# Performance work log

Hardware: AMD Instinct MI355X
Metric: run time of the kernel (lower is better)

Reference implementation:

```python
import jax, jax.numpy as jnp
import numpy as np

E = 8          # num_experts
K = 2          # top-k
H = 768        # hidden_size
F = 4 * H      # FFN intermediate (expansion_factor=4)
B, S = 2, 2048


def setup_inputs() -> dict:
    key = jax.random.key(0)
    ks = jax.random.split(key, 5)
    scale = 0.02
    return {
        "x": jax.random.normal(ks[0], (B, S, H), dtype=jnp.float32),
        "router_w": jax.random.normal(ks[1], (H, E), dtype=jnp.float32) * scale,
        "router_b": jnp.zeros((E,), dtype=jnp.float32),
        "w1": jax.random.normal(ks[2], (E, H, F), dtype=jnp.float32) * scale,
        "b1": jnp.zeros((E, F), dtype=jnp.float32),
        "w2": jax.random.normal(ks[3], (E, F, H), dtype=jnp.float32) * scale,
        "b2": jnp.zeros((E, H), dtype=jnp.float32),
    }


def reference(x, router_w, router_b, w1, b1, w2, b2):
    b, s, h = x.shape
    # Router
    scores = jnp.einsum("bsh,he->bse", x, router_w) + router_b
    probs = jax.nn.softmax(scores, axis=-1)                      # [b,s,E]
    top_probs, expert_ids = jax.lax.top_k(probs, K)              # [b,s,K]

    # Load-balance auxiliary loss (Switch-style)
    avg_probs = probs.mean(axis=(0, 1))                          # [E]
    top1 = jnp.argmax(probs, axis=-1).reshape(-1)                # [b*s]
    counts = jnp.zeros((E,), dtype=probs.dtype).at[top1].add(1.0)
    expert_freqs = counts / (b * s)
    bal_loss = 0.001 * jnp.dot(expert_freqs, avg_probs)

    # Normalize top-k gate weights
    norm_probs = top_probs / (top_probs.sum(axis=-1, keepdims=True) + 1e-9)  # [b,s,K]

    # Expert FFNs with ReLU^2 activation, computed per-expert (dense, then masked)
    h1 = jnp.einsum("bsh,ehf->ebsf", x, w1) + b1[:, None, None, :]
    h1 = jnp.square(jax.nn.relu(h1))
    h2 = jnp.einsum("ebsf,efh->ebsh", h1, w2) + b2[:, None, None, :]  # [E,b,s,H]

    # Combine: weight for expert e at token (b,s) = sum_k norm_probs * 1[ids_k == e]
    onehot = jax.nn.one_hot(expert_ids, E, dtype=x.dtype)        # [b,s,K,E]
    gate = jnp.einsum("bsk,bske->ebs", norm_probs, onehot)       # [E,b,s]
    out = jnp.einsum("ebs,ebsh->bsh", gate, h2)                  # [b,s,H]
    return out, bal_loss
```

## Files before the change

### kernel.cpp

```cpp
#include <hip/hip_runtime.h>
#include <hip/hip_bf16.h>
#include <stdint.h>

#define E_EXP 8
#define TOK   4096
#define HD    768
#define FD    3072
#define BK    64
#define CAP   8320

typedef __attribute__((ext_vector_type(8))) short bf16x8;
typedef __attribute__((ext_vector_type(4))) float f32x4;

__device__ __forceinline__ unsigned short f2bf(float f) {
  union { float f; unsigned u; } v; v.f = f;
  unsigned r = v.u + 0x7fffu + ((v.u >> 16) & 1u);
  return (unsigned short)(r >> 16);
}
__device__ __forceinline__ float bf2f(unsigned short u) {
  union { unsigned u; float f; } v; v.u = ((unsigned)u) << 16;
  return v.f;
}

__device__ __forceinline__ void gload_lds16(const void* g, void* l) {
  __builtin_amdgcn_global_load_lds(
      (const __attribute__((address_space(1))) unsigned int*)g,
      (__attribute__((address_space(3))) unsigned int*)l, 16, 0, 0);
}

__device__ __forceinline__ int xcd_swizzle(int orig, int nwg) {
  int xcd = orig & 7, base = orig >> 3;
  int q = nwg >> 3, r = nwg & 7;
  return (xcd < r ? xcd * (q + 1) : r * (q + 1) + (xcd - r) * q) + base;
}

__global__ __launch_bounds__(256) void router_kernel(
    const float* __restrict__ x, const float* __restrict__ rw,
    const float* __restrict__ rb, unsigned short* __restrict__ xb,
    float* __restrict__ probs, int* __restrict__ ids,
    float* __restrict__ gates)
{
  __shared__ float lrw[E_EXP * HD];
  for (int i = threadIdx.x; i < E_EXP * HD; i += 256) {
    int h = i >> 3, e = i & 7;
    lrw[e * HD + h] = rw[i];
  }
  __syncthreads();
  const int wave = threadIdx.x >> 6, lane = threadIdx.x & 63;
  const int t = blockIdx.x * 4 + wave;
  const float* xrow = x + (size_t)t * HD;
  float acc[8] = {0, 0, 0, 0, 0, 0, 0, 0};
#pragma unroll
  for (int i = 0; i < HD / 64; ++i) {
    int h = i * 64 + lane;
    float xv = xrow[h];
    xb[(size_t)t * HD + h] = f2bf(xv);
#pragma unroll
    for (int e = 0; e < 8; ++e) acc[e] += xv * lrw[e * HD + h];
  }
#pragma unroll
  for (int d = 1; d < 64; d <<= 1) {
#pragma unroll
    for (int e = 0; e < 8; ++e) acc[e] += __shfl_xor(acc[e], d);
  }
  if (lane == 0) {
    float p[8]; float m = -1e30f, sum = 0.f;
#pragma unroll
    for (int e = 0; e < 8; ++e) { p[e] = acc[e] + rb[e]; m = fmaxf(m, p[e]); }
#pragma unroll
    for (int e = 0; e < 8; ++e) { p[e] = __expf(p[e] - m); sum += p[e]; }
    float inv = 1.f / sum;
#pragma unroll
    for (int e = 0; e < 8; ++e) p[e] *= inv;
    int i1 = 0;
#pragma unroll
    for (int e = 1; e < 8; ++e) if (p[e] > p[i1]) i1 = e;
    int i2 = (i1 == 0) ? 1 : 0;
#pragma unroll
    for (int e = 0; e < 8; ++e) if (e != i1 && p[e] > p[i2]) i2 = e;
    ids[t * 2] = i1; ids[t * 2 + 1] = i2;
    float den = 1.f / (p[i1] + p[i2] + 1e-9f);
    gates[t * 2] = p[i1] * den; gates[t * 2 + 1] = p[i2] * den;
#pragma unroll
    for (int e = 0; e < 8; ++e) probs[t * 8 + e] = p[e];
  }
}

#define W1_TILES (E_EXP * (FD / 32) * (HD / 32))
#define W2_TILES (E_EXP * (HD / 32) * (FD / 32))
__global__ __launch_bounds__(256) void transpose_kernel(
    const float* __restrict__ w1, unsigned short* __restrict__ w1t,
    const float* __restrict__ w2, unsigned short* __restrict__ w2t)
{
  __shared__ float tile[32][33];
  int id = blockIdx.x;
  const float* W; unsigned short* Wt; int Kd, Nd;
  if (id < W1_TILES) {
    W = w1; Wt = w1t; Kd = HD; Nd = FD;
  } else {
    id -= W1_TILES; W = w2; Wt = w2t; Kd = FD; Nd = HD;
  }
  const int nx = Nd / 32;
  const int e = id / (nx * (Kd / 32));
  const int rem = id % (nx * (Kd / 32));
  const int n0 = (rem % nx) * 32, k0 = (rem / nx) * 32;

  const int ci = threadIdx.x & 31, ri = threadIdx.x >> 5;
  const float* src = W + ((size_t)e * Kd + k0) * Nd + n0;
#pragma unroll
  for (int i = 0; i < 32; i += 8)
    tile[ri + i][ci] = src[(size_t)(ri + i) * Nd + ci];
  __syncthreads();
  unsigned short* dst = Wt + ((size_t)e * Nd + n0) * Kd + k0;
  const int co = (threadIdx.x & 15) * 2, ro = threadIdx.x >> 4;
#pragma unroll
  for (int i = 0; i < 32; i += 16) {
    int r = ro + i;
    unsigned v = (unsigned)f2bf(tile[co][r]) | ((unsigned)f2bf(tile[co + 1][r]) << 16);
    *(unsigned*)&dst[(size_t)r * Kd + co] = v;
  }
}

__global__ __launch_bounds__(256) void stats_kernel(
    const int* __restrict__ ids, const float* __restrict__ probs,
    int* __restrict__ meta, float* __restrict__ loss_out)
{
  __shared__ int cnt[8], top1c[8];
  __shared__ float wsum[4][8];
  if (threadIdx.x < 8) { cnt[threadIdx.x] = 0; top1c[threadIdx.x] = 0; }
  __syncthreads();
  float local[8] = {0, 0, 0, 0, 0, 0, 0, 0};
  for (int t = threadIdx.x; t < TOK; t += 256) {
    int e0 = ids[2 * t], e1 = ids[2 * t + 1];
    atomicAdd(&cnt[e0], 1); atomicAdd(&cnt[e1], 1); atomicAdd(&top1c[e0], 1);
    const float4* pr = (const float4*)&probs[(size_t)t * 8];
    float4 a = pr[0], b = pr[1];
    local[0] += a.x; local[1] += a.y; local[2] += a.z; local[3] += a.w;
    local[4] += b.x; local[5] += b.y; local[6] += b.z; local[7] += b.w;
  }
#pragma unroll
  for (int d = 1; d < 64; d <<= 1) {
#pragma unroll
    for (int e = 0; e < 8; ++e) local[e] += __shfl_xor(local[e], d);
  }
  const int wave = threadIdx.x >> 6, lane = threadIdx.x & 63;
  if (lane == 0) {
#pragma unroll
    for (int e = 0; e < 8; ++e) wsum[wave][e] = local[e];
  }
  __syncthreads();
  if (threadIdx.x == 0) {
    int total = 0, nt1 = 0;
    for (int e = 0; e < 8; ++e) {
      int c = cnt[e];
      meta[e] = c;
      meta[16 + e] = total;
      int t1 = (c + 127) >> 7;
      for (int i = 0; i < t1; ++i) { meta[64 + nt1 * 2] = e; meta[64 + nt1 * 2 + 1] = total + i * 128; ++nt1; }
      total += c;
    }
    meta[32] = nt1;
    float loss = 0.f;
    for (int e = 0; e < 8; ++e) {
      float psum = wsum[0][e] + wsum[1][e] + wsum[2][e] + wsum[3][e];
      loss += ((float)top1c[e] / 4096.f) * (psum / 4096.f);
    }
    loss_out[0] = 0.001f * loss;
  }
}

__global__ __launch_bounds__(256) void scatter_kernel(
    const int* __restrict__ ids, int* __restrict__ meta,
    int* __restrict__ token_list, int* __restrict__ pos_list)
{
  __shared__ int lcnt[8];
  __shared__ int lbase[8];
  if (threadIdx.x < 8) lcnt[threadIdx.x] = 0;
  __syncthreads();
  const int t = blockIdx.x * 256 + threadIdx.x;
  const int e0 = ids[t * 2], e1 = ids[t * 2 + 1];
  const int s0 = atomicAdd(&lcnt[e0], 1);
  const int s1 = atomicAdd(&lcnt[e1], 1);
  __syncthreads();
  if (threadIdx.x < 8)
    lbase[threadIdx.x] = atomicAdd(&meta[24 + threadIdx.x], lcnt[threadIdx.x]);
  __syncthreads();
  int p0 = meta[16 + e0] + lbase[e0] + s0;
  int p1 = meta[16 + e1] + lbase[e1] + s1;
  token_list[p0] = t; pos_list[t * 2] = p0;
  token_list[p1] = t; pos_list[t * 2 + 1] = p1;
}

template<int BM, int BN, int MODE, int NW, int NKP>
__global__ __launch_bounds__(NW * 64, 4) void moe_gemm(
    const unsigned short* __restrict__ A,
    const unsigned short* __restrict__ Bw,
    const float* __restrict__ bias,
    const int* __restrict__ token_list,
    const int* __restrict__ meta,
    unsigned short* __restrict__ Cout,
    const int Kdim, const int NN)
{
  const int NY = NN / BN;
  const int wgid = xcd_swizzle(blockIdx.x, gridDim.x);
  const int mt = wgid / (NY * NKP);
  const int slot = wgid - mt * (NY * NKP);
  const int ny = slot % NY;
  const int kp = slot / NY;
  const int nt_total = meta[32];
  if (mt >= nt_total) return;
  const int* tmap = meta + 64;
  const int e = tmap[mt * 2], arow0 = tmap[mt * 2 + 1];
  const int ne_end = meta[16 + e] + meta[e];
  const int n0 = ny * BN;
  const int KLEN = Kdim / NKP;
  const int kbeg = kp * KLEN;
  unsigned short* Cp = Cout + (size_t)kp * CAP * NN;

  __shared__ unsigned short lA[BM * BK];
  __shared__ unsigned short lB[BN * BK];

  const int tid = threadIdx.x;
  const int wave = tid >> 6, lane = tid & 63;
  constexpr int WC_N = NW / 2;
  const int wr = wave / WC_N, wc = wave % WC_N;
  constexpr int WROWS = BM / 2;
  constexpr int WCOLS = BN / WC_N;
  constexpr int FM = WROWS / 16, FN = WCOLS / 16;
  constexpr int NCA = (BM / 8) / NW;
  constexpr int NCB = (BN / 8) / NW;

  const int kswz = ((lane & 7) ^ ((lane >> 3) & 7)) * 8;

  size_t aSrc[NCA];
#pragma unroll
  for (int i = 0; i < NCA; ++i) {
    int c = wave + i * NW;
    int r = c * 8 + (lane >> 3);
    int grow = (MODE == 0) ? token_list[arow0 + r] : (arow0 + r);
    aSrc[i] = (size_t)grow * Kdim + kbeg + kswz;
  }
  size_t bSrc[NCB];
#pragma unroll
  for (int i = 0; i < NCB; ++i) {
    int c = wave + i * NW;
    int n = n0 + c * 8 + (lane >> 3);
    bSrc[i] = ((size_t)e * NN + n) * Kdim + kbeg + kswz;
  }

  f32x4 acc[FM][FN] = {};

  for (int k0 = 0; k0 < KLEN; k0 += BK) {
#pragma unroll
    for (int i = 0; i < NCA; ++i)
      gload_lds16(A + aSrc[i] + k0, &lA[(wave + i * NW) * 512]);
#pragma unroll
    for (int i = 0; i < NCB; ++i)
      gload_lds16(Bw + bSrc[i] + k0, &lB[(wave + i * NW) * 512]);
    __syncthreads();
#pragma unroll
    for (int kk = 0; kk < BK; kk += 32) {
      bf16x8 af[FM], bfr[FN];
      const int lc = (kk >> 3) + (lane >> 4);
#pragma unroll
      for (int m2 = 0; m2 < FM; ++m2) {
        int row = wr * WROWS + m2 * 16 + (lane & 15);
        af[m2] = *(const bf16x8*)&lA[row * BK + ((lc ^ (row & 7)) << 3)];
      }
#pragma unroll
      for (int n2 = 0; n2 < FN; ++n2) {
        int row = wc * WCOLS + n2 * 16 + (lane & 15);
        bfr[n2] = *(const bf16x8*)&lB[row * BK + ((lc ^ (row & 7)) << 3)];
      }
#pragma unroll
      for (int m2 = 0; m2 < FM; ++m2)
#pragma unroll
        for (int n2 = 0; n2 < FN; ++n2)
          acc[m2][n2] = __builtin_amdgcn_mfma_f32_16x16x32_bf16(
              af[m2], bfr[n2], acc[m2][n2], 0, 0, 0);
    }
    __syncthreads();
  }

  const float* be = bias + (size_t)e * NN;
#pragma unroll
  for (int m2 = 0; m2 < FM; ++m2) {
    const int lr = wr * WROWS + m2 * 16 + (lane >> 4) * 4;
#pragma unroll
    for (int n2 = 0; n2 < FN; ++n2) {
      const int col = n0 + wc * WCOLS + n2 * 16 + (lane & 15);
      const float bv = (kp == 0) ? be[col] : 0.f;
#pragma unroll
      for (int j = 0; j < 4; ++j) {
        const int arow = arow0 + lr + j;
        if (arow < ne_end) {
          float v = acc[m2][n2][j] + bv;
          if (MODE == 0) { v = fmaxf(v, 0.f); v = v * v; }
          Cp[(size_t)arow * NN + col] = f2bf(v);
        }
      }
    }
  }
}

__global__ __launch_bounds__(256) void combine_kernel(
    const unsigned short* __restrict__ h2, const int* __restrict__ pos_list,
    const float* __restrict__ gates, float* __restrict__ out)
{
  const unsigned short* h2b = h2 + (size_t)CAP * HD;
  const int wave = threadIdx.x >> 6, lane = threadIdx.x & 63;
  const int t = blockIdx.x * 4 + wave;
  const int p0 = pos_list[2 * t], p1 = pos_list[2 * t + 1];
  const float g0 = gates[2 * t], g1 = gates[2 * t + 1];
  const unsigned short* r0a = h2  + (size_t)p0 * HD;
  const unsigned short* r0b = h2b + (size_t)p0 * HD;
  const unsigned short* r1a = h2  + (size_t)p1 * HD;
  const unsigned short* r1b = h2b + (size_t)p1 * HD;
  float* o = out + (size_t)t * HD;
#pragma unroll
  for (int i = 0; i < 3; ++i) {
    int h = i * 256 + lane * 4;
    ushort4 a0 = *(const ushort4*)&r0a[h];
    ushort4 b0 = *(const ushort4*)&r0b[h];
    ushort4 a1 = *(const ushort4*)&r1a[h];
    ushort4 b1 = *(const ushort4*)&r1b[h];
    float4 o4;
    o4.x = g0 * (bf2f(a0.x) + bf2f(b0.x)) + g1 * (bf2f(a1.x) + bf2f(b1.x));
    o4.y = g0 * (bf2f(a0.y) + bf2f(b0.y)) + g1 * (bf2f(a1.y) + bf2f(b1.y));
    o4.z = g0 * (bf2f(a0.z) + bf2f(b0.z)) + g1 * (bf2f(a1.z) + bf2f(b1.z));
    o4.w = g0 * (bf2f(a0.w) + bf2f(b0.w)) + g1 * (bf2f(a1.w) + bf2f(b1.w));
    *(float4*)&o[h] = o4;
  }
}

extern "C" void kernel_launch(void* const* d_in, const int* in_sizes, int n_in,
                              void* d_out, int out_size, void* d_ws, size_t ws_size,
                              hipStream_t stream)
{
  (void)in_sizes; (void)n_in; (void)ws_size; (void)out_size;
  const float* x  = (const float*)d_in[0];
  const float* rw = (const float*)d_in[1];
  const float* rb = (const float*)d_in[2];
  const float* w1 = (const float*)d_in[3];
  const float* b1 = (const float*)d_in[4];
  const float* w2 = (const float*)d_in[5];
  const float* b2 = (const float*)d_in[6];
  float* out = (float*)d_out;

  char* ws = (char*)d_ws;
  size_t off = 0;
  auto alloc = [&](size_t bytes) {
    off = (off + 255) & ~(size_t)255;
    void* p = ws + off;
    off += bytes;
    return p;
  };
  unsigned short* xb  = (unsigned short*)alloc((size_t)TOK * HD * 2);
  unsigned short* w1t = (unsigned short*)alloc((size_t)E_EXP * FD * HD * 2);
  unsigned short* w2t = (unsigned short*)alloc((size_t)E_EXP * HD * FD * 2);
  unsigned short* h1  = (unsigned short*)alloc((size_t)CAP * FD * 2);
  unsigned short* h2  = (unsigned short*)alloc((size_t)2 * CAP * HD * 2);
  int*   token_list = (int*)alloc(CAP * 4);
  int*   pos_list   = (int*)alloc((size_t)TOK * 2 * 4);
  int*   ids        = (int*)alloc((size_t)TOK * 2 * 4);
  float* gates      = (float*)alloc((size_t)TOK * 2 * 4);
  float* probs      = (float*)alloc((size_t)TOK * 8 * 4);
  int*   meta       = (int*)alloc(1024 * 4);
  char*  ctrl       = (char*)token_list;
  size_t ctrl_bytes = (ws + off) - ctrl;

  hipMemsetAsync(ctrl, 0, ctrl_bytes, stream);

  router_kernel<<<TOK / 4, 256, 0, stream>>>(x, rw, rb, xb, probs, ids, gates);
  transpose_kernel<<<W1_TILES + W2_TILES, 256, 0, stream>>>(w1, w1t, w2, w2t);
  stats_kernel<<<1, 256, 0, stream>>>(ids, probs, meta, out + (size_t)TOK * HD);
  scatter_kernel<<<TOK / 256, 256, 0, stream>>>(ids, meta, token_list, pos_list);
  moe_gemm<128, 128, 0, 4, 1><<<71 * (FD / 128), 256, 0, stream>>>(
      xb, w1t, b1, token_list, meta, h1, HD, FD);
  moe_gemm<128, 128, 1, 4, 2><<<71 * (HD / 128) * 2, 256, 0, stream>>>(
      h1, w2t, b2, token_list, meta, h2, FD, HD);
  combine_kernel<<<TOK / 4, 256, 0, stream>>>(h2, pos_list, gates, out);
}
```

Baseline: 201.8 us.

## Double-buffer LDS tiles in grouped expert GEMM to overlap loads with MFMA

Splits the A and B LDS tiles into two buffers and restructures the K loop so the global-to-LDS load for the next tile is issued before the MFMA work on the current tile. One barrier per iteration, preceded by an explicit vmcnt wait, replaces the two __syncthreads. The goal is to hide global memory latency behind matrix math. In exchange LDS use per block doubles, which can lower occupancy, and skipping the compiler's lgkmcnt wait before the barrier risks a read/write race on the buffer being refilled.

After: 255.5 us. 1.27x slower.

```diff
diff --git a/kernel.cpp b/kernel.cpp
--- a/kernel.cpp
+++ b/kernel.cpp
@@ -217,8 +217,8 @@
   const int kbeg = kp * KLEN;
   unsigned short* Cp = Cout + (size_t)kp * CAP * NN;
 
-  __shared__ unsigned short lA[BM * BK];
-  __shared__ unsigned short lB[BN * BK];
+  __shared__ unsigned short lA[2][BM * BK];
+  __shared__ unsigned short lB[2][BN * BK];
 
   const int tid = threadIdx.x;
   const int wave = tid >> 6, lane = tid & 63;
@@ -250,14 +250,16 @@
 
   f32x4 acc[FM][FN] = {};
 
-  for (int k0 = 0; k0 < KLEN; k0 += BK) {
+  auto STAGE = [&](int buf, int k0) {
 #pragma unroll
     for (int i = 0; i < NCA; ++i)
-      gload_lds16(A + aSrc[i] + k0, &lA[(wave + i * NW) * 512]);
+      gload_lds16(A + aSrc[i] + k0, &lA[buf][(wave + i * NW) * 512]);
 #pragma unroll
     for (int i = 0; i < NCB; ++i)
-      gload_lds16(Bw + bSrc[i] + k0, &lB[(wave + i * NW) * 512]);
-    __syncthreads();
+      gload_lds16(Bw + bSrc[i] + k0, &lB[buf][(wave + i * NW) * 512]);
+  };
+
+  auto COMPUTE = [&](int buf) {
 #pragma unroll
     for (int kk = 0; kk < BK; kk += 32) {
       bf16x8 af[FM], bfr[FN];
@@ -265,12 +267,12 @@
 #pragma unroll
       for (int m2 = 0; m2 < FM; ++m2) {
         int row = wr * WROWS + m2 * 16 + (lane & 15);
-        af[m2] = *(const bf16x8*)&lA[row * BK + ((lc ^ (row & 7)) << 3)];
+        af[m2] = *(const bf16x8*)&lA[buf][row * BK + ((lc ^ (row & 7)) << 3)];
       }
 #pragma unroll
       for (int n2 = 0; n2 < FN; ++n2) {
         int row = wc * WCOLS + n2 * 16 + (lane & 15);
-        bfr[n2] = *(const bf16x8*)&lB[row * BK + ((lc ^ (row & 7)) << 3)];
+        bfr[n2] = *(const bf16x8*)&lB[buf][row * BK + ((lc ^ (row & 7)) << 3)];
       }
 #pragma unroll
       for (int m2 = 0; m2 < FM; ++m2)
@@ -279,8 +281,21 @@
           acc[m2][n2] = __builtin_amdgcn_mfma_f32_16x16x32_bf16(
               af[m2], bfr[n2], acc[m2][n2], 0, 0, 0);
     }
-    __syncthreads();
-  }
+  };
+
+  const int NT = KLEN / BK;
+  STAGE(0, 0);
+  asm volatile("s_waitcnt vmcnt(0)" ::: "memory");
+  __builtin_amdgcn_s_barrier();
+  int cur = 0;
+  for (int t = 0; t < NT - 1; ++t) {
+    STAGE(cur ^ 1, (t + 1) * BK);
+    COMPUTE(cur);
+    asm volatile("s_waitcnt vmcnt(0)" ::: "memory");
+    __builtin_amdgcn_s_barrier();
+    cur ^= 1;
+  }
+  COMPUTE(cur);
 
   const float* be = bias + (size_t)e * NN;
 #pragma unroll
```

## Fuse stats and scatter kernels, raise split-K to three for second GEMM

Applied to the files above, without the earlier changes.

Merges the routing stats and scatter kernels into one 1024-thread single-block kernel, which removes a launch and the global atomics but serialises the scatter onto one workgroup. The second expert GEMM now splits K three ways instead of two, giving more workgroups to fill the GPU at the cost of an extra partial-output buffer. The combine kernel sums all three partials. The occupancy hint for the GEMM is also raised from 4 to 5 waves per SIMD, which may tighten the register budget.

Measured after the change: 331.2 us. 64.1% more time.

```diff
diff --git a/kernel.cpp b/kernel.cpp
--- a/kernel.cpp
+++ b/kernel.cpp
@@ -8,6 +8,7 @@
 #define FD    3072
 #define BK    64
 #define CAP   8320
+#define NKP2  3
 
 typedef __attribute__((ext_vector_type(8))) short bf16x8;
 typedef __attribute__((ext_vector_type(4))) float f32x4;
@@ -121,16 +122,19 @@
   }
 }
 
-__global__ __launch_bounds__(256) void stats_kernel(
+__global__ __launch_bounds__(1024) void stats_scatter_kernel(
     const int* __restrict__ ids, const float* __restrict__ probs,
-    int* __restrict__ meta, float* __restrict__ loss_out)
-{
-  __shared__ int cnt[8], top1c[8];
-  __shared__ float wsum[4][8];
-  if (threadIdx.x < 8) { cnt[threadIdx.x] = 0; top1c[threadIdx.x] = 0; }
+    const float* __restrict__ gates, int* __restrict__ meta,
+    int* __restrict__ token_list, int* __restrict__ pos_list,
+    float* __restrict__ loss_out)
+{
+  __shared__ int cnt[8], top1c[8], cur[8];
+  __shared__ float wsum[16][8];
+  const int tid = threadIdx.x;
+  if (tid < 8) { cnt[tid] = 0; top1c[tid] = 0; cur[tid] = 0; }
   __syncthreads();
   float local[8] = {0, 0, 0, 0, 0, 0, 0, 0};
-  for (int t = threadIdx.x; t < TOK; t += 256) {
+  for (int t = tid; t < TOK; t += 1024) {
     int e0 = ids[2 * t], e1 = ids[2 * t + 1];
     atomicAdd(&cnt[e0], 1); atomicAdd(&cnt[e1], 1); atomicAdd(&top1c[e0], 1);
     const float4* pr = (const float4*)&probs[(size_t)t * 8];
@@ -143,13 +147,13 @@
 #pragma unroll
     for (int e = 0; e < 8; ++e) local[e] += __shfl_xor(local[e], d);
   }
-  const int wave = threadIdx.x >> 6, lane = threadIdx.x & 63;
+  const int wave = tid >> 6, lane = tid & 63;
   if (lane == 0) {
 #pragma unroll
     for (int e = 0; e < 8; ++e) wsum[wave][e] = local[e];
   }
   __syncthreads();
-  if (threadIdx.x == 0) {
+  if (tid == 0) {
     int total = 0, nt1 = 0;
     for (int e = 0; e < 8; ++e) {
       int c = cnt[e];
@@ -162,37 +166,26 @@
     meta[32] = nt1;
     float loss = 0.f;
     for (int e = 0; e < 8; ++e) {
-      float psum = wsum[0][e] + wsum[1][e] + wsum[2][e] + wsum[3][e];
+      float psum = 0.f;
+      for (int w = 0; w < 16; ++w) psum += wsum[w][e];
       loss += ((float)top1c[e] / 4096.f) * (psum / 4096.f);
     }
     loss_out[0] = 0.001f * loss;
   }
-}
-
-__global__ __launch_bounds__(256) void scatter_kernel(
-    const int* __restrict__ ids, int* __restrict__ meta,
-    int* __restrict__ token_list, int* __restrict__ pos_list)
-{
-  __shared__ int lcnt[8];
-  __shared__ int lbase[8];
-  if (threadIdx.x < 8) lcnt[threadIdx.x] = 0;
-  __syncthreads();
-  const int t = blockIdx.x * 256 + threadIdx.x;
-  const int e0 = ids[t * 2], e1 = ids[t * 2 + 1];
-  const int s0 = atomicAdd(&lcnt[e0], 1);
-  const int s1 = atomicAdd(&lcnt[e1], 1);
-  __syncthreads();
-  if (threadIdx.x < 8)
-    lbase[threadIdx.x] = atomicAdd(&meta[24 + threadIdx.x], lcnt[threadIdx.x]);
-  __syncthreads();
-  int p0 = meta[16 + e0] + lbase[e0] + s0;
-  int p1 = meta[16 + e1] + lbase[e1] + s1;
-  token_list[p0] = t; pos_list[t * 2] = p0;
-  token_list[p1] = t; pos_list[t * 2 + 1] = p1;
+  __syncthreads();
+  for (int t = tid; t < TOK; t += 1024) {
+    int e0 = ids[2 * t], e1 = ids[2 * t + 1];
+    int s0 = atomicAdd(&cur[e0], 1);
+    int s1 = atomicAdd(&cur[e1], 1);
+    int p0 = meta[16 + e0] + s0;
+    int p1 = meta[16 + e1] + s1;
+    token_list[p0] = t; pos_list[2 * t] = p0;
+    token_list[p1] = t; pos_list[2 * t + 1] = p1;
+  }
 }
 
 template<int BM, int BN, int MODE, int NW, int NKP>
-__global__ __launch_bounds__(NW * 64, 4) void moe_gemm(
+__global__ __launch_bounds__(NW * 64, 5) void moe_gemm(
     const unsigned short* __restrict__ A,
     const unsigned short* __restrict__ Bw,
     const float* __restrict__ bias,
@@ -307,28 +300,25 @@
     const unsigned short* __restrict__ h2, const int* __restrict__ pos_list,
     const float* __restrict__ gates, float* __restrict__ out)
 {
-  const unsigned short* h2b = h2 + (size_t)CAP * HD;
   const int wave = threadIdx.x >> 6, lane = threadIdx.x & 63;
   const int t = blockIdx.x * 4 + wave;
   const int p0 = pos_list[2 * t], p1 = pos_list[2 * t + 1];
   const float g0 = gates[2 * t], g1 = gates[2 * t + 1];
-  const unsigned short* r0a = h2  + (size_t)p0 * HD;
-  const unsigned short* r0b = h2b + (size_t)p0 * HD;
-  const unsigned short* r1a = h2  + (size_t)p1 * HD;
-  const unsigned short* r1b = h2b + (size_t)p1 * HD;
   float* o = out + (size_t)t * HD;
 #pragma unroll
   for (int i = 0; i < 3; ++i) {
     int h = i * 256 + lane * 4;
-    ushort4 a0 = *(const ushort4*)&r0a[h];
-    ushort4 b0 = *(const ushort4*)&r0b[h];
-    ushort4 a1 = *(const ushort4*)&r1a[h];
-    ushort4 b1 = *(const ushort4*)&r1b[h];
-    float4 o4;
-    o4.x = g0 * (bf2f(a0.x) + bf2f(b0.x)) + g1 * (bf2f(a1.x) + bf2f(b1.x));
-    o4.y = g0 * (bf2f(a0.y) + bf2f(b0.y)) + g1 * (bf2f(a1.y) + bf2f(b1.y));
-    o4.z = g0 * (bf2f(a0.z) + bf2f(b0.z)) + g1 * (bf2f(a1.z) + bf2f(b1.z));
-    o4.w = g0 * (bf2f(a0.w) + bf2f(b0.w)) + g1 * (bf2f(a1.w) + bf2f(b1.w));
+    float4 o4 = {0.f, 0.f, 0.f, 0.f};
+#pragma unroll
+    for (int kp = 0; kp < NKP2; ++kp) {
+      const unsigned short* base = h2 + (size_t)kp * CAP * HD;
+      ushort4 a = *(const ushort4*)&base[(size_t)p0 * HD + h];
+      ushort4 b = *(const ushort4*)&base[(size_t)p1 * HD + h];
+      o4.x += g0 * bf2f(a.x) + g1 * bf2f(b.x);
+      o4.y += g0 * bf2f(a.y) + g1 * bf2f(b.y);
+      o4.z += g0 * bf2f(a.z) + g1 * bf2f(b.z);
+      o4.w += g0 * bf2f(a.w) + g1 * bf2f(b.w);
+    }
     *(float4*)&o[h] = o4;
   }
 }
@@ -359,7 +349,7 @@
   unsigned short* w1t = (unsigned short*)alloc((size_t)E_EXP * FD * HD * 2);
   unsigned short* w2t = (unsigned short*)alloc((size_t)E_EXP * HD * FD * 2);
   unsigned short* h1  = (unsigned short*)alloc((size_t)CAP * FD * 2);
-  unsigned short* h2  = (unsigned short*)alloc((size_t)2 * CAP * HD * 2);
+  unsigned short* h2  = (unsigned short*)alloc((size_t)NKP2 * CAP * HD * 2);
   int*   token_list = (int*)alloc(CAP * 4);
   int*   pos_list   = (int*)alloc((size_t)TOK * 2 * 4);
   int*   ids        = (int*)alloc((size_t)TOK * 2 * 4);
@@ -373,11 +363,11 @@
 
   router_kernel<<<TOK / 4, 256, 0, stream>>>(x, rw, rb, xb, probs, ids, gates);
   transpose_kernel<<<W1_TILES + W2_TILES, 256, 0, stream>>>(w1, w1t, w2, w2t);
-  stats_kernel<<<1, 256, 0, stream>>>(ids, probs, meta, out + (size_t)TOK * HD);
-  scatter_kernel<<<TOK / 256, 256, 0, stream>>>(ids, meta, token_list, pos_list);
+  stats_scatter_kernel<<<1, 1024, 0, stream>>>(ids, probs, gates, meta,
+      token_list, pos_list, out + (size_t)TOK * HD);
   moe_gemm<128, 128, 0, 4, 1><<<71 * (FD / 128), 256, 0, stream>>>(
       xb, w1t, b1, token_list, meta, h1, HD, FD);
-  moe_gemm<128, 128, 1, 4, 2><<<71 * (HD / 128) * 2, 256, 0, stream>>>(
+  moe_gemm<128, 128, 1, 4, NKP2><<<71 * (HD / 128) * NKP2, 256, 0, stream>>>(
       h1, w2t, b2, token_list, meta, h2, FD, HD);
   combine_kernel<<<TOK / 4, 256, 0, stream>>>(h2, pos_list, gates, out);
 }
```
